# Kernel optimization log

Hardware: AMD Instinct MI355X
Metric: run time of the kernel (lower is better)

## Reference

```python
import jax, jax.numpy as jnp
import numpy as np

B, HF, WF = 16, 32, 32
DIM, NH = 1024, 16
HD = DIM // NH  # 64


def axial_freqs(H, W, head_dim):
    # RotaryEmbedding(dim=head_dim//4, freqs_for='pixel', max_freq=H*W)
    d = head_dim // 4  # rotary dim per axis
    base = jnp.linspace(1.0, (H * W) / 2.0, d // 2) * jnp.pi  # [d//2]
    posH = jnp.linspace(-1.0, 1.0, H)
    posW = jnp.linspace(-1.0, 1.0, W)
    fH = jnp.repeat(posH[:, None] * base[None, :], 2, axis=-1)  # [H, d]
    fW = jnp.repeat(posW[:, None] * base[None, :], 2, axis=-1)  # [W, d]
    fH = jnp.broadcast_to(fH[:, None, :], (H, W, d))
    fW = jnp.broadcast_to(fW[None, :, :], (H, W, d))
    return jnp.concatenate([fH, fW], axis=-1)  # [H, W, 2d] = [H, W, head_dim//2]


def rotate_half(x):
    # interleaved pair rotation: (x1, x2) -> (-x2, x1)
    xr = x.reshape(*x.shape[:-1], -1, 2)
    x1, x2 = xr[..., 0], xr[..., 1]
    return jnp.stack([-x2, x1], axis=-1).reshape(x.shape)


def apply_rotary(freqs, t):
    # t: [B, h, H, W, hd]; freqs: [H, W, rot_dim]
    rd = freqs.shape[-1]
    t_rot, t_pass = t[..., :rd], t[..., rd:]
    t_rot = t_rot * jnp.cos(freqs) + rotate_half(t_rot) * jnp.sin(freqs)
    return jnp.concatenate([t_rot, t_pass], axis=-1)


def setup_inputs() -> dict:
    key = jax.random.key(0)
    k1, k2, k3 = jax.random.split(key, 3)
    s = 1.0 / np.sqrt(DIM)
    return {
        "x": jax.random.normal(k1, (B, HF * WF, DIM), jnp.float32),
        "w_qkv": jax.random.normal(k2, (3 * DIM, DIM), jnp.float32) * s,
        "w_proj": jax.random.normal(k3, (DIM, DIM), jnp.float32) * s,
        "b_proj": jnp.zeros((DIM,), jnp.float32),
    }


def reference(x, w_qkv, w_proj, b_proj):
    freqs = axial_freqs(HF, WF, HD)
    qkv = x @ w_qkv.T  # [B, N, 3*DIM]
    q, k, v = jnp.split(qkv, 3, axis=-1)

    def to_grid(t):  # [B, N, DIM] -> [B, h, H, W, hd]
        return t.reshape(B, HF, WF, NH, HD).transpose(0, 3, 1, 2, 4)

    q, k, v = to_grid(q), to_grid(k), to_grid(v)
    q = apply_rotary(freqs, q)
    k = apply_rotary(freqs, k)
    N = HF * WF
    q = q.reshape(B, NH, N, HD)
    k = k.reshape(B, NH, N, HD)
    v = v.reshape(B, NH, N, HD)

    scale = 1.0 / np.sqrt(HD)
    attn = jax.nn.softmax(jnp.einsum('bhnd,bhmd->bhnm', q, k) * scale, axis=-1)
    out = jnp.einsum('bhnm,bhmd->bhnd', attn, v)  # [B, h, N, hd]
    out = out.transpose(0, 2, 1, 3).reshape(B, N, DIM)
    return out @ w_proj.T + b_proj
```

## Files before the change

### kernel.cpp

```cpp
#include <hip/hip_runtime.h>
#include <hip/hip_bf16.h>
#include <math.h>

typedef __bf16 bf16;
typedef bf16 bf16x4 __attribute__((ext_vector_type(4)));
typedef bf16 bf16x8 __attribute__((ext_vector_type(8)));
typedef float f32x4 __attribute__((ext_vector_type(4)));

#define MFMA16(a, b, c) __builtin_amdgcn_mfma_f32_16x16x32_bf16((a), (b), (c), 0, 0, 0)

#define QSCALE 0.18033688011112042f

__device__ __forceinline__ void async16(const void* g, void* l) {
  __builtin_amdgcn_global_load_lds(
      (const __attribute__((address_space(1))) void*)g,
      (__attribute__((address_space(3))) void*)l, 16, 0, 0);
}

__global__ __launch_bounds__(256) void f2b_kernel(const float* __restrict__ in,
                                                  bf16* __restrict__ out, int n) {
  int i = (blockIdx.x * 256 + threadIdx.x) * 4;
  if (i >= n) return;
  f32x4 v = *(const f32x4*)(in + i);
  bf16x4 o = {(bf16)v[0], (bf16)v[1], (bf16)v[2], (bf16)v[3]};
  *(bf16x4*)(out + i) = o;
}

__global__ __launch_bounds__(256) void table_kernel(float* __restrict__ cosT,
                                                    float* __restrict__ sinT) {
  int idx = blockIdx.x * 256 + threadIdx.x;
  if (idx >= 1024 * 32) return;
  int n = idx >> 5, d = idx & 31;
  int hf = n >> 5, wf = n & 31;
  int bi = (d & 15) >> 1;
  float base = (1.0f + 73.0f * bi) * 3.14159265358979323846f;
  int p = (d < 16) ? hf : wf;
  float pos = (2.0f * (float)p - 31.0f) * (1.0f / 31.0f);
  float f = pos * base;
  cosT[idx] = cosf(f);
  sinT[idx] = sinf(f);
}

template <int EPI, int NBN>
__global__ __launch_bounds__(512, 2) void gemm_bt(
    const bf16* __restrict__ A, const bf16* __restrict__ W,
    bf16* __restrict__ oq, bf16* __restrict__ okk, bf16* __restrict__ ovt,
    const float* __restrict__ cosT, const float* __restrict__ sinT,
    float* __restrict__ outF, const float* __restrict__ bias) {
  constexpr int K = 1024;
  constexpr int NT = K / 64;
  __shared__ bf16 As[2][256 * 64];
  __shared__ bf16 Bs[2][256 * 64];

  const int tid = threadIdx.x;
  const int lane = tid & 63;
  const int wid = tid >> 6;
  const int lo = lane & 15, hi = lane >> 4;
  const int wm = wid >> 2;
  const int wn = wid & 3;

  const int wg = blockIdx.x;
  const int xcd = wg & 7;
  const int i = wg >> 3;
  const int bm = xcd * 8 + i / NBN;
  const int bn = i % NBN;

  const bf16* Ab = A + (size_t)bm * 256 * K;
  const bf16* Wb = W + (size_t)bn * 256 * K;

  const f32x4 fzero = {0.f, 0.f, 0.f, 0.f};
  f32x4 acc[8][4];
#pragma unroll
  for (int i2 = 0; i2 < 8; ++i2)
#pragma unroll
    for (int j = 0; j < 4; ++j) acc[i2][j] = fzero;

  size_t srcOff[4];
  int ldsOff[4];
#pragma unroll
  for (int i2 = 0; i2 < 4; ++i2) {
    const int c = i2 * 512 + tid;
    const int row = c >> 3, g = c & 7;
    const int gsrc = g ^ (row & 7);
    srcOff[i2] = (size_t)row * K + gsrc * 8;
    ldsOff[i2] = c * 8;
  }

  auto stageAll = [&](int buf, int kt) {
#pragma unroll
    for (int i2 = 0; i2 < 4; ++i2)
      async16(Ab + srcOff[i2] + kt * 64, &As[buf][ldsOff[i2]]);
#pragma unroll
    for (int i2 = 0; i2 < 4; ++i2)
      async16(Wb + srcOff[i2] + kt * 64, &Bs[buf][ldsOff[i2]]);
  };

  auto readA = [&](int buf, int mf, int s) -> bf16x8 {
    const int row = wm * 128 + mf * 16 + lo;
    const int col = (s * 32 + hi * 8) ^ ((row & 7) << 3);
    return *(const bf16x8*)&As[buf][row * 64 + col];
  };
  auto readB = [&](int buf, int nf, int s) -> bf16x8 {
    const int row = wn * 64 + nf * 16 + lo;
    const int col = (s * 32 + hi * 8) ^ ((row & 7) << 3);
    return *(const bf16x8*)&Bs[buf][row * 64 + col];
  };

  stageAll(0, 0);
  asm volatile("s_waitcnt vmcnt(0)");
  __builtin_amdgcn_s_barrier();

  int cur = 0;
  for (int kt = 0; kt < NT; ++kt) {
    bf16x8 bfr[4][2];
#pragma unroll
    for (int p = 0; p < 4; ++p) {
      bf16x8 af[2][2];
#pragma unroll
      for (int mi = 0; mi < 2; ++mi)
#pragma unroll
        for (int s = 0; s < 2; ++s) af[mi][s] = readA(cur, 2 * p + mi, s);
      if (p == 0) {
#pragma unroll
        for (int nf = 0; nf < 4; ++nf)
#pragma unroll
          for (int s = 0; s < 2; ++s) bfr[nf][s] = readB(cur, nf, s);
        if (kt < NT - 1) stageAll(cur ^ 1, kt + 1);
      }
      __builtin_amdgcn_s_barrier();
      __builtin_amdgcn_s_setprio(1);
#pragma unroll
      for (int mi = 0; mi < 2; ++mi)
#pragma unroll
        for (int nf = 0; nf < 4; ++nf)
#pragma unroll
          for (int s = 0; s < 2; ++s)
            acc[2 * p + mi][nf] = MFMA16(af[mi][s], bfr[nf][s], acc[2 * p + mi][nf]);
      __builtin_amdgcn_s_setprio(0);
      if (p == 3) asm volatile("s_waitcnt vmcnt(0)" ::: "memory");
      __builtin_amdgcn_s_barrier();
    }
    cur ^= 1;
  }

  const int rb0 = bm * 256 + wm * 128;
  const int jb0 = bn * 256 + wn * 64;

  if constexpr (EPI == 0) {
#pragma unroll
    for (int ac = 0; ac < 4; ++ac) {
      const int j = jb0 + ac * 16 + lo;
      const int which = j >> 10;
      const int f = j & 1023;
      const int h = f >> 6, d = f & 63;
#pragma unroll
      for (int ar = 0; ar < 8; ++ar) {
        const int rb = rb0 + ar * 16 + 4 * hi;
        f32x4 v = acc[ar][ac];
        if (which == 2) {
          const int b = rb >> 10, n0 = rb & 1023;
          bf16x4 pk = {(bf16)v[0], (bf16)v[1], (bf16)v[2], (bf16)v[3]};
          *(bf16x4*)(ovt + ((size_t)((b * 16 + h) * 64 + d)) * 1024 + n0) = pk;
        } else {
          bf16* dst = which ? okk : oq;
          const float sc = which ? 1.0f : QSCALE;
#pragma unroll
          for (int reg = 0; reg < 4; ++reg) {
            const int r = rb + reg;
            const int b = r >> 10, n = r & 1023;
            float val = v[reg];
            float res;
            if (d < 32) {
              float c = cosT[n * 32 + d];
              float s = sinT[n * 32 + d];
              float pp = __shfl_xor(val, 1);
              res = (d & 1) ? fmaf(val, c, pp * s) : fmaf(val, c, -(pp * s));
            } else {
              res = val;
            }
            dst[((size_t)((b * 16 + h) * 1024 + n)) * 64 + d] = (bf16)(res * sc);
          }
        }
      }
    }
  } else {
#pragma unroll
    for (int ac = 0; ac < 4; ++ac) {
      const int j = jb0 + ac * 16 + lo;
      const float bv = bias[j];
#pragma unroll
      for (int ar = 0; ar < 8; ++ar) {
        const int rb = rb0 + ar * 16 + 4 * hi;
#pragma unroll
        for (int reg = 0; reg < 4; ++reg)
          outF[(size_t)(rb + reg) * 1024 + j] = acc[ar][ac][reg] + bv;
      }
    }
  }
}

__global__ __launch_bounds__(512) void attn_fwd(const bf16* __restrict__ q,
                                                const bf16* __restrict__ k,
                                                const bf16* __restrict__ vt,
                                                bf16* __restrict__ o) {
  constexpr int LDK = 72;
  __shared__ bf16 Kt[2][64 * LDK];
  __shared__ bf16 Vt[2][64 * LDK];
  __shared__ bf16 Pt[8][16 * LDK];
  const int tid = threadIdx.x;
  const int lane = tid & 63, wid = tid >> 6;
  const int lo = lane & 15, hi = lane >> 4;
  const int j = blockIdx.x;
  const int bh = (j & 7) + ((j >> 6) << 3);
  const int qt = (j >> 3) & 7;
  const bf16* qg = q + (size_t)bh * 65536;
  const bf16* kg = k + (size_t)bh * 65536;
  const bf16* vg = vt + (size_t)bh * 65536;

  const int qrow = qt * 128 + wid * 16 + lo;
  const bf16x8 qf0 = *(const bf16x8*)(qg + (size_t)qrow * 64 + 8 * hi);
  const bf16x8 qf1 = *(const bf16x8*)(qg + (size_t)qrow * 64 + 8 * hi + 32);

  const f32x4 fzero = {0.f, 0.f, 0.f, 0.f};
  f32x4 of[4];
  float psum[4] = {0.f, 0.f, 0.f, 0.f};
#pragma unroll
  for (int i = 0; i < 4; ++i) of[i] = fzero;

  const int srow = tid >> 3;
  const int sc0 = (tid & 7) * 8;

  auto stageKV = [&](int buf, int kv) {
    *(bf16x8*)&Kt[buf][srow * LDK + sc0] =
        *(const bf16x8*)(kg + (size_t)(kv * 64 + srow) * 64 + sc0);
    *(bf16x8*)&Vt[buf][srow * LDK + sc0] =
        *(const bf16x8*)(vg + (size_t)srow * 1024 + kv * 64 + sc0);
  };

  stageKV(0, 0);
  __syncthreads();

  for (int kv = 0; kv < 16; ++kv) {
    const int cur = kv & 1;
    if (kv < 15) stageKV(cur ^ 1, kv + 1);

    f32x4 sf[4];
#pragma unroll
    for (int kf = 0; kf < 4; ++kf) {
      bf16x8 kb0 = *(const bf16x8*)&Kt[cur][(kf * 16 + lo) * LDK + 8 * hi];
      bf16x8 kb1 = *(const bf16x8*)&Kt[cur][(kf * 16 + lo) * LDK + 8 * hi + 32];
      f32x4 z = fzero;
      z = MFMA16(qf0, kb0, z);
      z = MFMA16(qf1, kb1, z);
      sf[kf] = z;
    }

#pragma unroll
    for (int kf = 0; kf < 4; ++kf) {
#pragma unroll
      for (int reg = 0; reg < 4; ++reg) {
        float p = __builtin_amdgcn_exp2f(sf[kf][reg]);
        psum[reg] += p;
        Pt[wid][(4 * hi + reg) * LDK + kf * 16 + lo] = (bf16)p;
      }
    }

    const bf16x8 pa0 = *(const bf16x8*)&Pt[wid][lo * LDK + 8 * hi];
    const bf16x8 pa1 = *(const bf16x8*)&Pt[wid][lo * LDK + 8 * hi + 32];
#pragma unroll
    for (int df = 0; df < 4; ++df) {
      bf16x8 vb0 = *(const bf16x8*)&Vt[cur][(df * 16 + lo) * LDK + 8 * hi];
      bf16x8 vb1 = *(const bf16x8*)&Vt[cur][(df * 16 + lo) * LDK + 8 * hi + 32];
      of[df] = MFMA16(pa0, vb0, of[df]);
      of[df] = MFMA16(pa1, vb1, of[df]);
    }
    __syncthreads();
  }

#pragma unroll
  for (int off = 1; off < 16; off <<= 1) {
#pragma unroll
    for (int reg = 0; reg < 4; ++reg) psum[reg] += __shfl_xor(psum[reg], off);
  }

  const int b = bh >> 4, h = bh & 15;
#pragma unroll
  for (int reg = 0; reg < 4; ++reg) {
    const int n = qt * 128 + wid * 16 + 4 * hi + reg;
    const float inv = 1.0f / psum[reg];
#pragma unroll
    for (int df = 0; df < 4; ++df)
      o[((size_t)(b * 1024 + n)) * 1024 + h * 64 + df * 16 + lo] =
          (bf16)(of[df][reg] * inv);
  }
}

extern "C" void kernel_launch(void* const* d_in, const int* in_sizes, int n_in,
                              void* d_out, int out_size, void* d_ws, size_t ws_size,
                              hipStream_t stream) {
  (void)in_sizes; (void)n_in; (void)out_size; (void)ws_size;
  const float* x = (const float*)d_in[0];
  const float* wqkv = (const float*)d_in[1];
  const float* wproj = (const float*)d_in[2];
  const float* bproj = (const float*)d_in[3];

  char* ws = (char*)d_ws;
  bf16* xb = (bf16*)(ws);
  bf16* wqb = (bf16*)(ws + 33554432);
  bf16* wpb = (bf16*)(ws + 39845888);
  float* cosT = (float*)(ws + 41943040);
  float* sinT = (float*)(ws + 42074112);
  bf16* qb = (bf16*)(ws + 42205184);
  bf16* kb = (bf16*)(ws + 75759616);
  bf16* vtb = (bf16*)(ws + 109314048);

  f2b_kernel<<<16384, 256, 0, stream>>>(x, xb, 16 * 1024 * 1024);
  f2b_kernel<<<3072, 256, 0, stream>>>(wqkv, wqb, 3 * 1024 * 1024);
  f2b_kernel<<<1024, 256, 0, stream>>>(wproj, wpb, 1024 * 1024);
  table_kernel<<<128, 256, 0, stream>>>(cosT, sinT);

  gemm_bt<0, 12><<<768, 512, 0, stream>>>(xb, wqb, qb, kb, vtb, cosT, sinT,
                                          nullptr, nullptr);
  attn_fwd<<<2048, 512, 0, stream>>>(qb, kb, vtb, xb);
  gemm_bt<1, 4><<<256, 512, 0, stream>>>(xb, wpb, nullptr, nullptr, nullptr,
                                         nullptr, nullptr, (float*)d_out, bproj);
}
```

Before: 313.9 us.

## Pipeline GEMM main loop as a 4-slot ring of K=32 slices

Replaces the double-buffered K=64 main loop with a four-slot LDS ring of K=32 slices. Loads run two slices ahead and use counted vmcnt waits, so there is one barrier per slice instead of draining all loads each tile. All A and B fragments for a slice are read at once before the MFMA burst. Total LDS stays the same, with a new swizzle for 32-wide rows. The risk is more barriers per K and more register pressure from holding 12 fragments.

```diff
diff --git a/kernel.cpp b/kernel.cpp
--- a/kernel.cpp
+++ b/kernel.cpp
@@ -48,9 +48,8 @@
     const float* __restrict__ cosT, const float* __restrict__ sinT,
     float* __restrict__ outF, const float* __restrict__ bias) {
   constexpr int K = 1024;
-  constexpr int NT = K / 64;
-  __shared__ bf16 As[2][256 * 64];
-  __shared__ bf16 Bs[2][256 * 64];
+  __shared__ bf16 As[4][256 * 32];
+  __shared__ bf16 Bs[4][256 * 32];
 
   const int tid = threadIdx.x;
   const int lane = tid & 63;
@@ -75,73 +74,75 @@
 #pragma unroll
     for (int j = 0; j < 4; ++j) acc[i2][j] = fzero;
 
-  size_t srcOff[4];
-  int ldsOff[4];
-#pragma unroll
-  for (int i2 = 0; i2 < 4; ++i2) {
+  size_t srcOff[2];
+  int ldsOff[2];
+#pragma unroll
+  for (int i2 = 0; i2 < 2; ++i2) {
     const int c = i2 * 512 + tid;
-    const int row = c >> 3, g = c & 7;
-    const int gsrc = g ^ (row & 7);
+    const int row = c >> 2, g = c & 3;
+    const int gsrc = g ^ ((row >> 1) & 3);
     srcOff[i2] = (size_t)row * K + gsrc * 8;
     ldsOff[i2] = c * 8;
   }
 
-  auto stageAll = [&](int buf, int kt) {
-#pragma unroll
-    for (int i2 = 0; i2 < 4; ++i2)
-      async16(Ab + srcOff[i2] + kt * 64, &As[buf][ldsOff[i2]]);
-#pragma unroll
-    for (int i2 = 0; i2 < 4; ++i2)
-      async16(Wb + srcOff[i2] + kt * 64, &Bs[buf][ldsOff[i2]]);
+  auto stageSlot = [&](int slot, int kh) {
+#pragma unroll
+    for (int i2 = 0; i2 < 2; ++i2)
+      async16(Ab + srcOff[i2] + kh * 32, &As[slot][ldsOff[i2]]);
+#pragma unroll
+    for (int i2 = 0; i2 < 2; ++i2)
+      async16(Wb + srcOff[i2] + kh * 32, &Bs[slot][ldsOff[i2]]);
   };
 
-  auto readA = [&](int buf, int mf, int s) -> bf16x8 {
-    const int row = wm * 128 + mf * 16 + lo;
-    const int col = (s * 32 + hi * 8) ^ ((row & 7) << 3);
-    return *(const bf16x8*)&As[buf][row * 64 + col];
+  auto compute = [&](int slot) {
+    bf16x8 af[8], bf[4];
+#pragma unroll
+    for (int mf = 0; mf < 8; ++mf) {
+      const int row = wm * 128 + mf * 16 + lo;
+      const int g = hi ^ ((row >> 1) & 3);
+      af[mf] = *(const bf16x8*)&As[slot][row * 32 + g * 8];
+    }
+#pragma unroll
+    for (int nf = 0; nf < 4; ++nf) {
+      const int row = wn * 64 + nf * 16 + lo;
+      const int g = hi ^ ((row >> 1) & 3);
+      bf[nf] = *(const bf16x8*)&Bs[slot][row * 32 + g * 8];
+    }
+    __builtin_amdgcn_s_setprio(1);
+#pragma unroll
+    for (int mf = 0; mf < 8; ++mf)
+#pragma unroll
+      for (int nf = 0; nf < 4; ++nf)
+        acc[mf][nf] = MFMA16(af[mf], bf[nf], acc[mf][nf]);
+    __builtin_amdgcn_s_setprio(0);
   };
-  auto readB = [&](int buf, int nf, int s) -> bf16x8 {
-    const int row = wn * 64 + nf * 16 + lo;
-    const int col = (s * 32 + hi * 8) ^ ((row & 7) << 3);
-    return *(const bf16x8*)&Bs[buf][row * 64 + col];
-  };
-
-  stageAll(0, 0);
-  asm volatile("s_waitcnt vmcnt(0)");
+
+  stageSlot(0, 0);
+  stageSlot(1, 1);
+
+  for (int kt = 0; kt < 7; ++kt) {
+#pragma unroll
+    for (int ph = 0; ph < 4; ++ph) {
+      stageSlot((ph + 2) & 3, kt * 4 + ph + 2);
+      asm volatile("s_waitcnt vmcnt(8)" ::: "memory");
+      __builtin_amdgcn_s_barrier();
+      compute(ph);
+    }
+  }
+  stageSlot(2, 30);
+  asm volatile("s_waitcnt vmcnt(8)" ::: "memory");
   __builtin_amdgcn_s_barrier();
-
-  int cur = 0;
-  for (int kt = 0; kt < NT; ++kt) {
-    bf16x8 bfr[4][2];
-#pragma unroll
-    for (int p = 0; p < 4; ++p) {
-      bf16x8 af[2][2];
-#pragma unroll
-      for (int mi = 0; mi < 2; ++mi)
-#pragma unroll
-        for (int s = 0; s < 2; ++s) af[mi][s] = readA(cur, 2 * p + mi, s);
-      if (p == 0) {
-#pragma unroll
-        for (int nf = 0; nf < 4; ++nf)
-#pragma unroll
-          for (int s = 0; s < 2; ++s) bfr[nf][s] = readB(cur, nf, s);
-        if (kt < NT - 1) stageAll(cur ^ 1, kt + 1);
-      }
-      __builtin_amdgcn_s_barrier();
-      __builtin_amdgcn_s_setprio(1);
-#pragma unroll
-      for (int mi = 0; mi < 2; ++mi)
-#pragma unroll
-        for (int nf = 0; nf < 4; ++nf)
-#pragma unroll
-          for (int s = 0; s < 2; ++s)
-            acc[2 * p + mi][nf] = MFMA16(af[mi][s], bfr[nf][s], acc[2 * p + mi][nf]);
-      __builtin_amdgcn_s_setprio(0);
-      if (p == 3) asm volatile("s_waitcnt vmcnt(0)" ::: "memory");
-      __builtin_amdgcn_s_barrier();
-    }
-    cur ^= 1;
-  }
+  compute(0);
+  stageSlot(3, 31);
+  asm volatile("s_waitcnt vmcnt(8)" ::: "memory");
+  __builtin_amdgcn_s_barrier();
+  compute(1);
+  asm volatile("s_waitcnt vmcnt(4)" ::: "memory");
+  __builtin_amdgcn_s_barrier();
+  compute(2);
+  asm volatile("s_waitcnt vmcnt(0)" ::: "memory");
+  __builtin_amdgcn_s_barrier();
+  compute(3);
 
   const int rb0 = bm * 256 + wm * 128;
   const int jb0 = bn * 256 + wn * 64;
```

Result: faster. 302.3 us (-3.7%).
